# Performance work log

Measured on AMD Instinct MI355X. Metric: run time of the kernel, lower is better.

## Reference

```python
import jax, jax.numpy as jnp
import numpy as np


def setup_inputs() -> dict:
    key = jax.random.key(0)
    k1, k2 = jax.random.split(key)
    b, c, h, w = 8, 256, 96, 192
    x = jax.random.normal(k1, (b, c, h, w), dtype=jnp.float32)
    y = jax.random.normal(k2, (b, c, h, w), dtype=jnp.float32)
    return {"x": x, "y": y, "max_displacement": 4}


def _correlation(x, y, md):
    # x, y: [B, C, H, W]. Output: [B, K*K, H, W], K = 2*md+1.
    b, c, h, w = x.shape
    K = 2 * md + 1
    # zero-pad y spatially so out-of-bounds displacements contribute 0
    yp = jnp.pad(y, ((0, 0), (0, 0), (md, md), (md, md)))
    # fixed small loop over K*K displacements (81 for md=4)
    outs = [
        jnp.einsum('bchw,bchw->bhw', x, yp[:, :, di:di + h, dj:dj + w])
        for di in range(K) for dj in range(K)
    ]
    out = jnp.stack(outs, axis=1)  # [B, K*K, H, W]
    return out / c


def reference(x, y, max_displacement):
    return _correlation(x, y, max_displacement)
```

## Files before the change

### kernel.cpp

```cpp
#include <hip/hip_runtime.h>
#include <hip/hip_bf16.h>
#include <stdint.h>


using f32x4 = __attribute__((ext_vector_type(4))) float;
using s16x4 = __attribute__((ext_vector_type(4))) short;
using u16x4 = __attribute__((ext_vector_type(4))) unsigned short;

#define C_DIM 256
#define H_DIM 96
#define W_DIM 192
#define HWSZ  (H_DIM * W_DIM)
#define MD 4
#define KD 9
#define CHUNK 32
#define HR 8
#define NTHR 512
#define WTILES 12
#define HQ 12
#define SUB_B 128
#define YROW_B (16 * SUB_B)
#define XROW_B (8 * SUB_B)
#define XBASE  (16 * YROW_B)
#define LDS_BYTES (XBASE + 8 * XROW_B)

static __device__ __forceinline__ unsigned short bf16b(float f) {
  __bf16 h = (__bf16)f;
  unsigned short s; __builtin_memcpy(&s, &h, 2); return s;
}

static __device__ __forceinline__ s16x4 tr16(uint32_t addr) {
  s16x4 d;
  asm volatile("ds_read_b64_tr_b16 %0, %1" : "=v"(d) : "v"(addr));
  return d;
}

__global__ __launch_bounds__(NTHR, 4)
void corr_mfma(const float* __restrict__ xg, const float* __restrict__ yg,
               float* __restrict__ outg) {
  __shared__ __align__(16) char smem[LDS_BYTES];

  const int bid = blockIdx.x;
  const int b   = bid & 7;
  const int rem = bid >> 3;
  const int wt  = rem / HQ;
  const int hq  = rem - wt * HQ;
  const int w0  = wt * 16;
  const int h0  = hq * HR;

  const int tid  = threadIdx.x;
  const int lane = tid & 63;
  const int wv   = tid >> 6;
  const int hi   = lane >> 4;
  const int lm   = lane & 15;

  const uint32_t sbase = (uint32_t)(uintptr_t)&smem[0];

  uint32_t goffY[6], loffY[6], goffX[2], loffX[2];
  uint32_t vmaskY = 0;
#pragma unroll
  for (int i = 0; i < 6; ++i) {
    const int qid = i * NTHR + tid;
    const int q = qid % 6;
    const int c = (qid / 6) % CHUNK;
    const int r = qid / 192;
    const int hg = h0 + r - MD;
    const int sg = w0 - MD + 4 * q;
    const bool ok = (hg >= 0) && (hg < H_DIM) && (sg >= 0) && (sg < W_DIM);
    if (ok) vmaskY |= (1u << i);
    goffY[i] = ok ? (uint32_t)(((b * C_DIM + c) * H_DIM + hg) * W_DIM + sg) : 0u;
    const int s = 4 * q;
    loffY[i] = r * YROW_B + (s >> 4) * (8 * SUB_B) + (c >> 2) * SUB_B
             + (c & 3) * 32 + (s & 15) * 2;
  }
#pragma unroll
  for (int i = 0; i < 2; ++i) {
    const int qid = i * NTHR + tid;
    const int q = qid & 3;
    const int c = (qid >> 2) & 31;
    const int r = qid >> 7;
    goffX[i] = (uint32_t)(((b * C_DIM + c) * H_DIM + (h0 + r)) * W_DIM + (w0 + 4 * q));
    loffX[i] = XBASE + r * XROW_B + (c >> 2) * SUB_B + (c & 3) * 32 + 8 * q;
  }

  f32x4 acc[KD][2];
#pragma unroll
  for (int di = 0; di < KD; ++di) {
    acc[di][0] = f32x4{0.f, 0.f, 0.f, 0.f};
    acc[di][1] = f32x4{0.f, 0.f, 0.f, 0.f};
  }

  const uint32_t abase = sbase + XBASE + wv * XROW_B + hi * SUB_B + lm * 8;
  const uint32_t bbase = sbase + wv * YROW_B + hi * SUB_B + lm * 8;

  for (int c0 = 0; c0 < C_DIM; c0 += CHUNK) {
    u16x4 wbuf[8];
#pragma unroll
    for (int i = 0; i < 6; ++i) {
      float4 v = make_float4(0.f, 0.f, 0.f, 0.f);
      if (vmaskY & (1u << i)) v = *(const float4*)(yg + goffY[i] + (uint32_t)c0 * HWSZ);
      wbuf[i] = u16x4{bf16b(v.x), bf16b(v.y), bf16b(v.z), bf16b(v.w)};
    }
#pragma unroll
    for (int i = 0; i < 2; ++i) {
      float4 v = *(const float4*)(xg + goffX[i] + (uint32_t)c0 * HWSZ);
      wbuf[6 + i] = u16x4{bf16b(v.x), bf16b(v.y), bf16b(v.z), bf16b(v.w)};
    }

    __syncthreads();
#pragma unroll
    for (int i = 0; i < 6; ++i) *(u16x4*)(smem + loffY[i]) = wbuf[i];
#pragma unroll
    for (int i = 0; i < 2; ++i) *(u16x4*)(smem + loffX[i]) = wbuf[6 + i];
    __syncthreads();

    s16x4 afr0 = tr16(abase);
    s16x4 afr1 = tr16(abase + 4 * SUB_B);
    s16x4 bc0 = tr16(bbase);
    s16x4 bc1 = tr16(bbase + 4 * SUB_B);
    s16x4 bc2 = tr16(bbase + 8 * SUB_B);
    s16x4 bc3 = tr16(bbase + 12 * SUB_B);
#pragma unroll
    for (int di = 0; di < KD; ++di) {
      s16x4 bn0, bn1, bn2, bn3;
      if (di < 8) {
        const uint32_t bb = bbase + (uint32_t)(di + 1) * YROW_B;
        bn0 = tr16(bb);
        bn1 = tr16(bb + 4 * SUB_B);
        bn2 = tr16(bb + 8 * SUB_B);
        bn3 = tr16(bb + 12 * SUB_B);
        asm volatile("s_waitcnt lgkmcnt(4)" ::: "memory");
      } else {
        asm volatile("s_waitcnt lgkmcnt(0)" ::: "memory");
      }
      __builtin_amdgcn_sched_barrier(0);
      acc[di][0] = __builtin_amdgcn_mfma_f32_16x16x16bf16_1k(afr0, bc0, acc[di][0], 0, 0, 0);
      acc[di][0] = __builtin_amdgcn_mfma_f32_16x16x16bf16_1k(afr1, bc1, acc[di][0], 0, 0, 0);
      acc[di][1] = __builtin_amdgcn_mfma_f32_16x16x16bf16_1k(afr0, bc2, acc[di][1], 0, 0, 0);
      acc[di][1] = __builtin_amdgcn_mfma_f32_16x16x16bf16_1k(afr1, bc3, acc[di][1], 0, 0, 0);
      if (di < 8) { bc0 = bn0; bc1 = bn1; bc2 = bn2; bc3 = bn3; }
    }
  }

  const int h = h0 + wv;
  const float scale = 1.f / 256.f;
#pragma unroll
  for (int di = 0; di < KD; ++di) {
#pragma unroll
    for (int t = 0; t < 2; ++t) {
#pragma unroll
      for (int rg = 0; rg < 4; ++rg) {
        const int m = hi * 4 + rg;
        const int dj = t * 16 + lm - m;
        if (0 <= dj && dj <= 8) {
          outg[((b * (KD * KD) + di * KD + dj) * H_DIM + h) * W_DIM + w0 + m] =
              acc[di][t][rg] * scale;
        }
      }
    }
  }
}

extern "C" void kernel_launch(void* const* d_in, const int* in_sizes, int n_in,
                              void* d_out, int out_size, void* d_ws, size_t ws_size,
                              hipStream_t stream) {
  const float* x = (const float*)d_in[0];
  const float* y = (const float*)d_in[1];
  float* out = (float*)d_out;
  (void)in_sizes; (void)n_in; (void)d_ws; (void)ws_size; (void)out_size;

  const int grid = 8 * HQ * WTILES;
  corr_mfma<<<dim3(grid), dim3(NTHR), 0, stream>>>(x, y, out);
}
```

Measured before the change: 139.4 us.

## Load x fragments directly to registers and double the channel chunk

The x tile no longer goes through LDS. Each lane loads its MFMA A-fragment straight from global memory with scalar loads and converts it to bf16 in registers. The channel chunk doubles to 64, which halves the number of block barriers, and the LDS transpose reads for y are double-buffered one displacement row ahead with eight reads in flight. In exchange, LDS use per block grows to 64 KB, which may lower the number of resident blocks per CU, and the x loads become narrower 4-byte accesses.

```diff
diff --git a/kernel.cpp b/kernel.cpp
--- a/kernel.cpp
+++ b/kernel.cpp
@@ -13,16 +13,16 @@
 #define HWSZ  (H_DIM * W_DIM)
 #define MD 4
 #define KD 9
-#define CHUNK 32
+#define CHUNK 64
+#define NCHUNK 4
 #define HR 8
 #define NTHR 512
 #define WTILES 12
 #define HQ 12
 #define SUB_B 128
-#define YROW_B (16 * SUB_B)
-#define XROW_B (8 * SUB_B)
-#define XBASE  (16 * YROW_B)
-#define LDS_BYTES (XBASE + 8 * XROW_B)
+#define YROW_B (32 * SUB_B)
+#define LDS_BYTES (16 * YROW_B)
+#define NYQ (16 * CHUNK * 6)
 
 static __device__ __forceinline__ unsigned short bf16b(float f) {
   __bf16 h = (__bf16)f;
@@ -34,6 +34,8 @@
   asm volatile("ds_read_b64_tr_b16 %0, %1" : "=v"(d) : "v"(addr));
   return d;
 }
+
+#define WAITLG(n) asm volatile("s_waitcnt lgkmcnt(" #n ")" ::: "memory")
 
 __global__ __launch_bounds__(NTHR, 4)
 void corr_mfma(const float* __restrict__ xg, const float* __restrict__ yg,
@@ -56,32 +58,27 @@
 
   const uint32_t sbase = (uint32_t)(uintptr_t)&smem[0];
 
-  uint32_t goffY[6], loffY[6], goffX[2], loffX[2];
+  uint32_t goffY[12], loffY[12];
   uint32_t vmaskY = 0;
 #pragma unroll
-  for (int i = 0; i < 6; ++i) {
+  for (int i = 0; i < 12; ++i) {
     const int qid = i * NTHR + tid;
     const int q = qid % 6;
     const int c = (qid / 6) % CHUNK;
-    const int r = qid / 192;
+    const int r = qid / 384;
     const int hg = h0 + r - MD;
     const int sg = w0 - MD + 4 * q;
     const bool ok = (hg >= 0) && (hg < H_DIM) && (sg >= 0) && (sg < W_DIM);
     if (ok) vmaskY |= (1u << i);
     goffY[i] = ok ? (uint32_t)(((b * C_DIM + c) * H_DIM + hg) * W_DIM + sg) : 0u;
     const int s = 4 * q;
-    loffY[i] = r * YROW_B + (s >> 4) * (8 * SUB_B) + (c >> 2) * SUB_B
+    loffY[i] = r * YROW_B + (s >> 4) * (16 * SUB_B) + (c >> 2) * SUB_B
              + (c & 3) * 32 + (s & 15) * 2;
   }
-#pragma unroll
-  for (int i = 0; i < 2; ++i) {
-    const int qid = i * NTHR + tid;
-    const int q = qid & 3;
-    const int c = (qid >> 2) & 31;
-    const int r = qid >> 7;
-    goffX[i] = (uint32_t)(((b * C_DIM + c) * H_DIM + (h0 + r)) * W_DIM + (w0 + 4 * q));
-    loffX[i] = XBASE + r * XROW_B + (c >> 2) * SUB_B + (c & 3) * 32 + 8 * q;
-  }
+
+  const int h = h0 + wv;
+  const uint32_t xbase =
+      (uint32_t)(((b * C_DIM + hi * 4) * H_DIM + h) * W_DIM + w0 + lm);
 
   f32x4 acc[KD][2];
 #pragma unroll
@@ -90,71 +87,92 @@
     acc[di][1] = f32x4{0.f, 0.f, 0.f, 0.f};
   }
 
-  const uint32_t abase = sbase + XBASE + wv * XROW_B + hi * SUB_B + lm * 8;
-  const uint32_t bbase = sbase + wv * YROW_B + hi * SUB_B + lm * 8;
+  const uint32_t bbase = sbase + (uint32_t)wv * YROW_B + hi * SUB_B + lm * 8;
 
-  for (int c0 = 0; c0 < C_DIM; c0 += CHUNK) {
-    u16x4 wbuf[8];
+  for (int t = 0; t < NCHUNK; ++t) {
+    const uint32_t co = (uint32_t)t * CHUNK * HWSZ;
+
+    u16x4 wbuf[12];
 #pragma unroll
-    for (int i = 0; i < 6; ++i) {
+    for (int i = 0; i < 12; ++i) {
       float4 v = make_float4(0.f, 0.f, 0.f, 0.f);
-      if (vmaskY & (1u << i)) v = *(const float4*)(yg + goffY[i] + (uint32_t)c0 * HWSZ);
+      if (vmaskY & (1u << i)) v = *(const float4*)(yg + goffY[i] + co);
       wbuf[i] = u16x4{bf16b(v.x), bf16b(v.y), bf16b(v.z), bf16b(v.w)};
     }
+    s16x4 afr[4];
 #pragma unroll
-    for (int i = 0; i < 2; ++i) {
-      float4 v = *(const float4*)(xg + goffX[i] + (uint32_t)c0 * HWSZ);
-      wbuf[6 + i] = u16x4{bf16b(v.x), bf16b(v.y), bf16b(v.z), bf16b(v.w)};
+    for (int kh = 0; kh < 4; ++kh) {
+      float xv0 = xg[xbase + co + (uint32_t)(kh * 16 + 0) * HWSZ];
+      float xv1 = xg[xbase + co + (uint32_t)(kh * 16 + 1) * HWSZ];
+      float xv2 = xg[xbase + co + (uint32_t)(kh * 16 + 2) * HWSZ];
+      float xv3 = xg[xbase + co + (uint32_t)(kh * 16 + 3) * HWSZ];
+      afr[kh][0] = (short)bf16b(xv0); afr[kh][1] = (short)bf16b(xv1);
+      afr[kh][2] = (short)bf16b(xv2); afr[kh][3] = (short)bf16b(xv3);
     }
 
     __syncthreads();
 #pragma unroll
-    for (int i = 0; i < 6; ++i) *(u16x4*)(smem + loffY[i]) = wbuf[i];
-#pragma unroll
-    for (int i = 0; i < 2; ++i) *(u16x4*)(smem + loffX[i]) = wbuf[6 + i];
+    for (int i = 0; i < 12; ++i) *(u16x4*)(smem + loffY[i]) = wbuf[i];
     __syncthreads();
 
-    s16x4 afr0 = tr16(abase);
-    s16x4 afr1 = tr16(abase + 4 * SUB_B);
-    s16x4 bc0 = tr16(bbase);
-    s16x4 bc1 = tr16(bbase + 4 * SUB_B);
-    s16x4 bc2 = tr16(bbase + 8 * SUB_B);
-    s16x4 bc3 = tr16(bbase + 12 * SUB_B);
-#pragma unroll
-    for (int di = 0; di < KD; ++di) {
-      s16x4 bn0, bn1, bn2, bn3;
-      if (di < 8) {
-        const uint32_t bb = bbase + (uint32_t)(di + 1) * YROW_B;
-        bn0 = tr16(bb);
-        bn1 = tr16(bb + 4 * SUB_B);
-        bn2 = tr16(bb + 8 * SUB_B);
-        bn3 = tr16(bb + 12 * SUB_B);
-        asm volatile("s_waitcnt lgkmcnt(4)" ::: "memory");
-      } else {
-        asm volatile("s_waitcnt lgkmcnt(0)" ::: "memory");
-      }
-      __builtin_amdgcn_sched_barrier(0);
-      acc[di][0] = __builtin_amdgcn_mfma_f32_16x16x16bf16_1k(afr0, bc0, acc[di][0], 0, 0, 0);
-      acc[di][0] = __builtin_amdgcn_mfma_f32_16x16x16bf16_1k(afr1, bc1, acc[di][0], 0, 0, 0);
-      acc[di][1] = __builtin_amdgcn_mfma_f32_16x16x16bf16_1k(afr0, bc2, acc[di][1], 0, 0, 0);
-      acc[di][1] = __builtin_amdgcn_mfma_f32_16x16x16bf16_1k(afr1, bc3, acc[di][1], 0, 0, 0);
-      if (di < 8) { bc0 = bn0; bc1 = bn1; bc2 = bn2; bc3 = bn3; }
-    }
+    s16x4 bsl[2][8];
+
+#define ISSUE_DI(di) { \
+    const uint32_t ba = bbase + (uint32_t)(di) * YROW_B; \
+    bsl[(di) & 1][0] = tr16(ba);            \
+    bsl[(di) & 1][1] = tr16(ba + 512);      \
+    bsl[(di) & 1][2] = tr16(ba + 1024);     \
+    bsl[(di) & 1][3] = tr16(ba + 1536);     \
+    bsl[(di) & 1][4] = tr16(ba + 2048);     \
+    bsl[(di) & 1][5] = tr16(ba + 2560);     \
+    bsl[(di) & 1][6] = tr16(ba + 3072);     \
+    bsl[(di) & 1][7] = tr16(ba + 3584); }
+
+#define DO_DI(di, lg) \
+    WAITLG(lg); __builtin_amdgcn_sched_barrier(0); \
+    acc[di][0] = __builtin_amdgcn_mfma_f32_16x16x16bf16_1k(afr[0], bsl[(di) & 1][0], acc[di][0], 0, 0, 0); \
+    acc[di][0] = __builtin_amdgcn_mfma_f32_16x16x16bf16_1k(afr[1], bsl[(di) & 1][1], acc[di][0], 0, 0, 0); \
+    acc[di][0] = __builtin_amdgcn_mfma_f32_16x16x16bf16_1k(afr[2], bsl[(di) & 1][2], acc[di][0], 0, 0, 0); \
+    acc[di][0] = __builtin_amdgcn_mfma_f32_16x16x16bf16_1k(afr[3], bsl[(di) & 1][3], acc[di][0], 0, 0, 0); \
+    acc[di][1] = __builtin_amdgcn_mfma_f32_16x16x16bf16_1k(afr[0], bsl[(di) & 1][4], acc[di][1], 0, 0, 0); \
+    acc[di][1] = __builtin_amdgcn_mfma_f32_16x16x16bf16_1k(afr[1], bsl[(di) & 1][5], acc[di][1], 0, 0, 0); \
+    acc[di][1] = __builtin_amdgcn_mfma_f32_16x16x16bf16_1k(afr[2], bsl[(di) & 1][6], acc[di][1], 0, 0, 0); \
+    acc[di][1] = __builtin_amdgcn_mfma_f32_16x16x16bf16_1k(afr[3], bsl[(di) & 1][7], acc[di][1], 0, 0, 0);
+
+    ISSUE_DI(0)
+    ISSUE_DI(1)
+    DO_DI(0, 8)
+    ISSUE_DI(2)
+    DO_DI(1, 8)
+    ISSUE_DI(3)
+    DO_DI(2, 8)
+    ISSUE_DI(4)
+    DO_DI(3, 8)
+    ISSUE_DI(5)
+    DO_DI(4, 8)
+    ISSUE_DI(6)
+    DO_DI(5, 8)
+    ISSUE_DI(7)
+    DO_DI(6, 8)
+    ISSUE_DI(8)
+    DO_DI(7, 8)
+    DO_DI(8, 0)
+#undef ISSUE_DI
+#undef DO_DI
   }
 
-  const int h = h0 + wv;
   const float scale = 1.f / 256.f;
 #pragma unroll
   for (int di = 0; di < KD; ++di) {
 #pragma unroll
-    for (int t = 0; t < 2; ++t) {
+    for (int tt = 0; tt < 2; ++tt) {
 #pragma unroll
       for (int rg = 0; rg < 4; ++rg) {
         const int m = hi * 4 + rg;
-        const int dj = t * 16 + lm - m;
+        const int dj = tt * 16 + lm - m;
         if (0 <= dj && dj <= 8) {
           outg[((b * (KD * KD) + di * KD + dj) * H_DIM + h) * W_DIM + w0 + m] =
-              acc[di][t][rg] * scale;
+              acc[di][tt][rg] * scale;
         }
       }
     }
```

Result: slower. 210.4 us (+50.9%).

## Remap MFMA tiles to 2 rows by 8 columns per wave for shared B fragments

Applied to the files above, without the earlier changes.

Each wave now owns a 2-row by 8-column output patch instead of one row by 16 columns. The 16 B columns (8 pixels plus 8 displacements) then fit a single 16-wide MFMA tile, and the two query rows share the y rows they need. This drops the MFMAs per chunk from 36 to 20 and also cuts the transposed LDS reads, at the cost of computing some wasted output entries per tile. LDS layouts and the global-load slots are rearranged to match, and setprio is raised around the MFMA burst.

```diff
diff --git a/kernel.cpp b/kernel.cpp
--- a/kernel.cpp
+++ b/kernel.cpp
@@ -14,15 +14,15 @@
 #define MD 4
 #define KD 9
 #define CHUNK 32
+#define NCHUNK 8
 #define HR 8
 #define NTHR 512
 #define WTILES 12
 #define HQ 12
-#define SUB_B 128
-#define YROW_B (16 * SUB_B)
-#define XROW_B (8 * SUB_B)
+#define YROW_B 2048
 #define XBASE  (16 * YROW_B)
-#define LDS_BYTES (XBASE + 8 * XROW_B)
+#define LDS_BYTES (XBASE + 8 * 1024)
+#define NSLOT 10
 
 static __device__ __forceinline__ unsigned short bf16b(float f) {
   __bf16 h = (__bf16)f;
@@ -34,6 +34,8 @@
   asm volatile("ds_read_b64_tr_b16 %0, %1" : "=v"(d) : "v"(addr));
   return d;
 }
+
+#define WAITLG(n) asm volatile("s_waitcnt lgkmcnt(" #n ")" ::: "memory")
 
 __global__ __launch_bounds__(NTHR, 4)
 void corr_mfma(const float* __restrict__ xg, const float* __restrict__ yg,
@@ -51,111 +53,123 @@
   const int tid  = threadIdx.x;
   const int lane = tid & 63;
   const int wv   = tid >> 6;
+  const int p    = wv >> 1;
+  const int wh   = wv & 1;
   const int hi   = lane >> 4;
   const int lm   = lane & 15;
 
   const uint32_t sbase = (uint32_t)(uintptr_t)&smem[0];
 
-  uint32_t goffY[6], loffY[6], goffX[2], loffX[2];
-  uint32_t vmaskY = 0;
+  uint32_t goff[NSLOT], loff[NSLOT];
+  uint32_t vmask = 0;
 #pragma unroll
-  for (int i = 0; i < 6; ++i) {
-    const int qid = i * NTHR + tid;
-    const int q = qid % 6;
-    const int c = (qid / 6) % CHUNK;
-    const int r = qid / 192;
-    const int hg = h0 + r - MD;
-    const int sg = w0 - MD + 4 * q;
-    const bool ok = (hg >= 0) && (hg < H_DIM) && (sg >= 0) && (sg < W_DIM);
-    if (ok) vmaskY |= (1u << i);
-    goffY[i] = ok ? (uint32_t)(((b * C_DIM + c) * H_DIM + hg) * W_DIM + sg) : 0u;
-    const int s = 4 * q;
-    loffY[i] = r * YROW_B + (s >> 4) * (8 * SUB_B) + (c >> 2) * SUB_B
-             + (c & 3) * 32 + (s & 15) * 2;
-  }
-#pragma unroll
-  for (int i = 0; i < 2; ++i) {
-    const int qid = i * NTHR + tid;
-    const int q = qid & 3;
-    const int c = (qid >> 2) & 31;
-    const int r = qid >> 7;
-    goffX[i] = (uint32_t)(((b * C_DIM + c) * H_DIM + (h0 + r)) * W_DIM + (w0 + 4 * q));
-    loffX[i] = XBASE + r * XROW_B + (c >> 2) * SUB_B + (c & 3) * 32 + 8 * q;
+  for (int i = 0; i < NSLOT; ++i) {
+    const int sid = i * NTHR + tid;
+    if (i < 8) {
+      const int r  = sid >> 8;
+      const int u  = sid & 255;
+      const int c  = u >> 3;
+      const int ph = (u >> 2) & 1;
+      const int qp = u & 3;
+      const int hg = h0 + r - MD;
+      const int sg = w0 - MD + 8 * ph + 4 * qp;
+      const bool ok = (hg >= 0) && (hg < H_DIM) && (sg >= 0) && (sg + 3 < W_DIM);
+      if (ok) vmask |= (1u << i);
+      goff[i] = ok ? (uint32_t)(((b * C_DIM + c) * H_DIM + hg) * W_DIM + sg) : 0u;
+      loff[i] = r * YROW_B + (c >> 2) * 256 + ph * 128 + (c & 3) * 32 + qp * 8;
+    } else {
+      const int v  = sid - 4096;
+      const int r8 = v >> 7;
+      const int u  = v & 127;
+      const int c  = u >> 2;
+      const int q  = u & 3;
+      vmask |= (1u << i);
+      goff[i] = (uint32_t)(((b * C_DIM + c) * H_DIM + (h0 + r8)) * W_DIM + (w0 + 4 * q));
+      loff[i] = XBASE + ((r8 >> 1) * 2 + (q >> 1)) * 1024 + (c >> 2) * 128
+              + (c & 3) * 32 + ((r8 & 1) * 8 + (q & 1) * 4) * 2;
+    }
   }
 
-  f32x4 acc[KD][2];
+  f32x4 acc[10];
 #pragma unroll
-  for (int di = 0; di < KD; ++di) {
-    acc[di][0] = f32x4{0.f, 0.f, 0.f, 0.f};
-    acc[di][1] = f32x4{0.f, 0.f, 0.f, 0.f};
-  }
+  for (int r = 0; r < 10; ++r) acc[r] = f32x4{0.f, 0.f, 0.f, 0.f};
 
-  const uint32_t abase = sbase + XBASE + wv * XROW_B + hi * SUB_B + lm * 8;
-  const uint32_t bbase = sbase + wv * YROW_B + hi * SUB_B + lm * 8;
+  const uint32_t abase = sbase + XBASE + (uint32_t)(p * 2 + wh) * 1024 + hi * 128 + lm * 8;
+  const uint32_t bbase = sbase + (uint32_t)(2 * p) * YROW_B + hi * 256 + wh * 128 + lm * 8;
 
-  for (int c0 = 0; c0 < C_DIM; c0 += CHUNK) {
-    u16x4 wbuf[8];
+  for (int t = 0; t < NCHUNK; ++t) {
+    const uint32_t co = (uint32_t)t * CHUNK * HWSZ;
+
+    u16x4 wbuf[NSLOT];
 #pragma unroll
-    for (int i = 0; i < 6; ++i) {
+    for (int i = 0; i < NSLOT; ++i) {
       float4 v = make_float4(0.f, 0.f, 0.f, 0.f);
-      if (vmaskY & (1u << i)) v = *(const float4*)(yg + goffY[i] + (uint32_t)c0 * HWSZ);
+      if (i < 8) {
+        if (vmask & (1u << i)) v = *(const float4*)(yg + goff[i] + co);
+      } else {
+        v = *(const float4*)(xg + goff[i] + co);
+      }
       wbuf[i] = u16x4{bf16b(v.x), bf16b(v.y), bf16b(v.z), bf16b(v.w)};
-    }
-#pragma unroll
-    for (int i = 0; i < 2; ++i) {
-      float4 v = *(const float4*)(xg + goffX[i] + (uint32_t)c0 * HWSZ);
-      wbuf[6 + i] = u16x4{bf16b(v.x), bf16b(v.y), bf16b(v.z), bf16b(v.w)};
     }
 
     __syncthreads();
 #pragma unroll
-    for (int i = 0; i < 6; ++i) *(u16x4*)(smem + loffY[i]) = wbuf[i];
-#pragma unroll
-    for (int i = 0; i < 2; ++i) *(u16x4*)(smem + loffX[i]) = wbuf[6 + i];
+    for (int i = 0; i < NSLOT; ++i) *(u16x4*)(smem + loff[i]) = wbuf[i];
     __syncthreads();
 
     s16x4 afr0 = tr16(abase);
-    s16x4 afr1 = tr16(abase + 4 * SUB_B);
-    s16x4 bc0 = tr16(bbase);
-    s16x4 bc1 = tr16(bbase + 4 * SUB_B);
-    s16x4 bc2 = tr16(bbase + 8 * SUB_B);
-    s16x4 bc3 = tr16(bbase + 12 * SUB_B);
-#pragma unroll
-    for (int di = 0; di < KD; ++di) {
-      s16x4 bn0, bn1, bn2, bn3;
-      if (di < 8) {
-        const uint32_t bb = bbase + (uint32_t)(di + 1) * YROW_B;
-        bn0 = tr16(bb);
-        bn1 = tr16(bb + 4 * SUB_B);
-        bn2 = tr16(bb + 8 * SUB_B);
-        bn3 = tr16(bb + 12 * SUB_B);
-        asm volatile("s_waitcnt lgkmcnt(4)" ::: "memory");
-      } else {
-        asm volatile("s_waitcnt lgkmcnt(0)" ::: "memory");
-      }
-      __builtin_amdgcn_sched_barrier(0);
-      acc[di][0] = __builtin_amdgcn_mfma_f32_16x16x16bf16_1k(afr0, bc0, acc[di][0], 0, 0, 0);
-      acc[di][0] = __builtin_amdgcn_mfma_f32_16x16x16bf16_1k(afr1, bc1, acc[di][0], 0, 0, 0);
-      acc[di][1] = __builtin_amdgcn_mfma_f32_16x16x16bf16_1k(afr0, bc2, acc[di][1], 0, 0, 0);
-      acc[di][1] = __builtin_amdgcn_mfma_f32_16x16x16bf16_1k(afr1, bc3, acc[di][1], 0, 0, 0);
-      if (di < 8) { bc0 = bn0; bc1 = bn1; bc2 = bn2; bc3 = bn3; }
-    }
+    s16x4 afr1 = tr16(abase + 512);
+    s16x4 bsl[2][2];
+
+#define ISSUE_R(r) { \
+    const uint32_t ba = bbase + (uint32_t)(r) * YROW_B; \
+    bsl[(r) & 1][0] = tr16(ba); \
+    bsl[(r) & 1][1] = tr16(ba + 1024); }
+
+#define DO_R(r, lg) \
+    WAITLG(lg); __builtin_amdgcn_sched_barrier(0); \
+    acc[r] = __builtin_amdgcn_mfma_f32_16x16x16bf16_1k(afr0, bsl[(r) & 1][0], acc[r], 0, 0, 0); \
+    acc[r] = __builtin_amdgcn_mfma_f32_16x16x16bf16_1k(afr1, bsl[(r) & 1][1], acc[r], 0, 0, 0);
+
+    __builtin_amdgcn_s_setprio(1);
+    ISSUE_R(0)
+    ISSUE_R(1)
+    DO_R(0, 2)
+    ISSUE_R(2)
+    DO_R(1, 2)
+    ISSUE_R(3)
+    DO_R(2, 2)
+    ISSUE_R(4)
+    DO_R(3, 2)
+    ISSUE_R(5)
+    DO_R(4, 2)
+    ISSUE_R(6)
+    DO_R(5, 2)
+    ISSUE_R(7)
+    DO_R(6, 2)
+    ISSUE_R(8)
+    DO_R(7, 2)
+    ISSUE_R(9)
+    DO_R(8, 2)
+    DO_R(9, 0)
+    __builtin_amdgcn_s_setprio(0);
+#undef ISSUE_R
+#undef DO_R
   }
 
-  const int h = h0 + wv;
   const float scale = 1.f / 256.f;
 #pragma unroll
-  for (int di = 0; di < KD; ++di) {
+  for (int r = 0; r < 10; ++r) {
 #pragma unroll
-    for (int t = 0; t < 2; ++t) {
-#pragma unroll
-      for (int rg = 0; rg < 4; ++rg) {
-        const int m = hi * 4 + rg;
-        const int dj = t * 16 + lm - m;
-        if (0 <= dj && dj <= 8) {
-          outg[((b * (KD * KD) + di * KD + dj) * H_DIM + h) * W_DIM + w0 + m] =
-              acc[di][t][rg] * scale;
-        }
+    for (int rg = 0; rg < 4; ++rg) {
+      const int m = hi * 4 + rg;
+      const int j = m >> 3;
+      const int w = m & 7;
+      const int di = r - j;
+      const int dj = lm - w;
+      if (0 <= di && di < KD && 0 <= dj && dj < KD) {
+        outg[((b * (KD * KD) + di * KD + dj) * H_DIM + (h0 + 2 * p + j)) * W_DIM
+             + (w0 + 8 * wh + w)] = acc[r][rg] * scale;
       }
     }
   }
```

New measurement: 147.0 us. +5.4%, slower.

## Double-buffer x via async global-to-LDS DMA and prefetch y one chunk ahead

Applied to the files above, without the earlier changes.

The x tile is now fetched with global_load_lds straight into one of two fp32 LDS buffers, issued two chunks ahead, instead of going through registers. The y tile for the next chunk is loaded into registers during the current chunk's MFMA work and converted and stored to LDS after a barrier. x is converted to bf16 at fragment-read time with eight scalar LDS reads instead of a transposed read. The aim is to overlap global memory latency with compute; in exchange LDS use grows and the occupancy hint drops from 4 to 3 blocks per CU.

```diff
diff --git a/kernel.cpp b/kernel.cpp
--- a/kernel.cpp
+++ b/kernel.cpp
@@ -6,6 +6,9 @@
 using f32x4 = __attribute__((ext_vector_type(4))) float;
 using s16x4 = __attribute__((ext_vector_type(4))) short;
 using u16x4 = __attribute__((ext_vector_type(4))) unsigned short;
+
+#define AS1 __attribute__((address_space(1)))
+#define AS3 __attribute__((address_space(3)))
 
 #define C_DIM 256
 #define H_DIM 96
@@ -14,15 +17,16 @@
 #define MD 4
 #define KD 9
 #define CHUNK 32
+#define NCHUNK 8
 #define HR 8
 #define NTHR 512
 #define WTILES 12
 #define HQ 12
 #define SUB_B 128
 #define YROW_B (16 * SUB_B)
-#define XROW_B (8 * SUB_B)
-#define XBASE  (16 * YROW_B)
-#define LDS_BYTES (XBASE + 8 * XROW_B)
+#define YBYTES (16 * YROW_B)
+#define XBUF_B 16384
+#define LDS_BYTES (YBYTES + 2 * XBUF_B)
 
 static __device__ __forceinline__ unsigned short bf16b(float f) {
   __bf16 h = (__bf16)f;
@@ -35,7 +39,7 @@
   return d;
 }
 
-__global__ __launch_bounds__(NTHR, 4)
+__global__ __launch_bounds__(NTHR, 3)
 void corr_mfma(const float* __restrict__ xg, const float* __restrict__ yg,
                float* __restrict__ outg) {
   __shared__ __align__(16) char smem[LDS_BYTES];
@@ -56,8 +60,8 @@
 
   const uint32_t sbase = (uint32_t)(uintptr_t)&smem[0];
 
-  uint32_t goffY[6], loffY[6], goffX[2], loffX[2];
-  uint32_t vmaskY = 0;
+  uint32_t goffY[6], loffY[6];
+  uint32_t vmY = 0;
 #pragma unroll
   for (int i = 0; i < 6; ++i) {
     const int qid = i * NTHR + tid;
@@ -67,20 +71,21 @@
     const int hg = h0 + r - MD;
     const int sg = w0 - MD + 4 * q;
     const bool ok = (hg >= 0) && (hg < H_DIM) && (sg >= 0) && (sg < W_DIM);
-    if (ok) vmaskY |= (1u << i);
+    if (ok) vmY |= (1u << i);
     goffY[i] = ok ? (uint32_t)(((b * C_DIM + c) * H_DIM + hg) * W_DIM + sg) : 0u;
     const int s = 4 * q;
     loffY[i] = r * YROW_B + (s >> 4) * (8 * SUB_B) + (c >> 2) * SUB_B
              + (c & 3) * 32 + (s & 15) * 2;
   }
-#pragma unroll
-  for (int i = 0; i < 2; ++i) {
-    const int qid = i * NTHR + tid;
-    const int q = qid & 3;
-    const int c = (qid >> 2) & 31;
-    const int r = qid >> 7;
-    goffX[i] = (uint32_t)(((b * C_DIM + c) * H_DIM + (h0 + r)) * W_DIM + (w0 + 4 * q));
-    loffX[i] = XBASE + r * XROW_B + (c >> 2) * SUB_B + (c & 3) * 32 + 8 * q;
+
+  uint32_t goffX[2];
+#pragma unroll
+  for (int j = 0; j < 2; ++j) {
+    const int u = j * NTHR + tid;
+    const int r = u >> 7;
+    const int c = (u >> 2) & 31;
+    const int sq = u & 3;
+    goffX[j] = (uint32_t)(((b * C_DIM + c) * H_DIM + (h0 + r)) * W_DIM + (w0 + 4 * sq));
   }
 
   f32x4 acc[KD][2];
@@ -90,32 +95,54 @@
     acc[di][1] = f32x4{0.f, 0.f, 0.f, 0.f};
   }
 
-  const uint32_t abase = sbase + XBASE + wv * XROW_B + hi * SUB_B + lm * 8;
   const uint32_t bbase = sbase + wv * YROW_B + hi * SUB_B + lm * 8;
-
-  for (int c0 = 0; c0 < C_DIM; c0 += CHUNK) {
-    u16x4 wbuf[8];
-#pragma unroll
-    for (int i = 0; i < 6; ++i) {
-      float4 v = make_float4(0.f, 0.f, 0.f, 0.f);
-      if (vmaskY & (1u << i)) v = *(const float4*)(yg + goffY[i] + (uint32_t)c0 * HWSZ);
-      wbuf[i] = u16x4{bf16b(v.x), bf16b(v.y), bf16b(v.z), bf16b(v.w)};
-    }
-#pragma unroll
-    for (int i = 0; i < 2; ++i) {
-      float4 v = *(const float4*)(xg + goffX[i] + (uint32_t)c0 * HWSZ);
-      wbuf[6 + i] = u16x4{bf16b(v.x), bf16b(v.y), bf16b(v.z), bf16b(v.w)};
-    }
-
-    __syncthreads();
-#pragma unroll
-    for (int i = 0; i < 6; ++i) *(u16x4*)(smem + loffY[i]) = wbuf[i];
-#pragma unroll
-    for (int i = 0; i < 2; ++i) *(u16x4*)(smem + loffX[i]) = wbuf[6 + i];
-    __syncthreads();
-
-    s16x4 afr0 = tr16(abase);
-    s16x4 afr1 = tr16(abase + 4 * SUB_B);
+  const int abase = wv * 512 + hi * 64 + lm;
+
+  AS3 char* lds = (AS3 char*)smem;
+
+#define XDMA(t) { \
+    const uint32_t co = (uint32_t)(t) * CHUNK * HWSZ; \
+    const uint32_t dst = YBYTES + (uint32_t)((t) & 1) * XBUF_B; \
+    _Pragma("unroll") \
+    for (int j = 0; j < 2; ++j) \
+      __builtin_amdgcn_global_load_lds((const AS1 void*)(xg + goffX[j] + co), \
+          (AS3 void*)(lds + dst + (uint32_t)(j * 8 + wv) * 1024), 16, 0, 0); \
+  }
+
+#define YLOAD(t) { \
+    const uint32_t co = (uint32_t)(t) * CHUNK * HWSZ; \
+    _Pragma("unroll") \
+    for (int i = 0; i < 6; ++i) { \
+      float4 v4 = make_float4(0.f, 0.f, 0.f, 0.f); \
+      if (vmY & (1u << i)) v4 = *(const float4*)(yg + goffY[i] + co); \
+      yv[i] = v4; \
+    } }
+
+  float4 yv[6];
+
+  XDMA(0)
+  YLOAD(0)
+#pragma unroll
+  for (int i = 0; i < 6; ++i)
+    *(u16x4*)(smem + loffY[i]) =
+        u16x4{bf16b(yv[i].x), bf16b(yv[i].y), bf16b(yv[i].z), bf16b(yv[i].w)};
+  XDMA(1)
+  YLOAD(1)
+  __syncthreads();
+
+  for (int t = 0; t < NCHUNK; ++t) {
+    const float* X = (const float*)(smem + YBYTES + (t & 1) * XBUF_B);
+    s16x4 afr0, afr1;
+    {
+      float a0 = X[abase],       a1 = X[abase + 16];
+      float a2 = X[abase + 32],  a3 = X[abase + 48];
+      float a4 = X[abase + 256], a5 = X[abase + 272];
+      float a6 = X[abase + 288], a7 = X[abase + 304];
+      afr0[0] = (short)bf16b(a0); afr0[1] = (short)bf16b(a1);
+      afr0[2] = (short)bf16b(a2); afr0[3] = (short)bf16b(a3);
+      afr1[0] = (short)bf16b(a4); afr1[1] = (short)bf16b(a5);
+      afr1[2] = (short)bf16b(a6); afr1[3] = (short)bf16b(a7);
+    }
     s16x4 bc0 = tr16(bbase);
     s16x4 bc1 = tr16(bbase + 4 * SUB_B);
     s16x4 bc2 = tr16(bbase + 8 * SUB_B);
@@ -140,6 +167,20 @@
       acc[di][1] = __builtin_amdgcn_mfma_f32_16x16x16bf16_1k(afr1, bc3, acc[di][1], 0, 0, 0);
       if (di < 8) { bc0 = bn0; bc1 = bn1; bc2 = bn2; bc3 = bn3; }
     }
+
+    __syncthreads();
+
+    if (t + 1 < NCHUNK) {
+#pragma unroll
+      for (int i = 0; i < 6; ++i)
+        *(u16x4*)(smem + loffY[i]) =
+            u16x4{bf16b(yv[i].x), bf16b(yv[i].y), bf16b(yv[i].z), bf16b(yv[i].w)};
+      if (t + 2 < NCHUNK) {
+        XDMA(t + 2)
+        YLOAD(t + 2)
+      }
+    }
+    __syncthreads();
   }
 
   const int h = h0 + wv;
```

Measured after the change: 189.9 us. 36.2% more time.
